# Performance work log

Measured on AMD Instinct MI355X. Metric: run time of the kernel, lower is better.

Reference implementation:

```python
import jax, jax.numpy as jnp
import numpy as np

D_MODEL, H, D_FF = 1024, 16, 4096
B, S = 2, 2048
EPS = 1e-6


def setup_inputs() -> dict:
    key = jax.random.key(0)
    ks = jax.random.split(key, 12)
    sc = 0.02
    p = lambda k, shape: (jax.random.normal(k, shape, dtype=jnp.float32) * sc)
    return {
        "x": jax.random.normal(ks[0], (B, S, D_MODEL), dtype=jnp.float32),
        "mask": jnp.ones((B, 1, 1, S), dtype=jnp.int32),
        "wq": p(ks[1], (D_MODEL, D_MODEL)), "bq": jnp.zeros((D_MODEL,), jnp.float32),
        "wk": p(ks[2], (D_MODEL, D_MODEL)), "bk": jnp.zeros((D_MODEL,), jnp.float32),
        "wv": p(ks[3], (D_MODEL, D_MODEL)), "bv": jnp.zeros((D_MODEL,), jnp.float32),
        "wo": p(ks[4], (D_MODEL, D_MODEL)), "bo": jnp.zeros((D_MODEL,), jnp.float32),
        "w1": p(ks[5], (D_FF, D_MODEL)), "b1": jnp.zeros((D_FF,), jnp.float32),
        "w2": p(ks[6], (D_MODEL, D_FF)), "b2": jnp.zeros((D_MODEL,), jnp.float32),
        "ln1_a": jnp.ones((D_MODEL,), jnp.float32), "ln1_b": jnp.zeros((D_MODEL,), jnp.float32),
        "ln2_a": jnp.ones((D_MODEL,), jnp.float32), "ln2_b": jnp.zeros((D_MODEL,), jnp.float32),
    }


def _layernorm(x, alpha, beta):
    # Matches the torch module: unbiased std (ddof=1), eps added to std (not var).
    mean = jnp.mean(x, axis=-1, keepdims=True)
    std = jnp.std(x, axis=-1, keepdims=True, ddof=1)
    return alpha * (x - mean) / (std + EPS) + beta


def _mha(x, mask, wq, bq, wk, bk, wv, bv, wo, bo):
    b, s, d = x.shape
    d_k = d // H
    # torch Linear: y = x @ W^T + b
    q = (x @ wq.T + bq).reshape(b, s, H, d_k).transpose(0, 2, 1, 3)
    k = (x @ wk.T + bk).reshape(b, s, H, d_k).transpose(0, 2, 1, 3)
    v = (x @ wv.T + bv).reshape(b, s, H, d_k).transpose(0, 2, 1, 3)
    scores = jnp.einsum("bhqd,bhkd->bhqk", q, k) / jnp.sqrt(jnp.float32(d_k))
    scores = jnp.where(mask == 0, jnp.float32(-1e9), scores)
    attn = jax.nn.softmax(scores, axis=-1)
    out = jnp.einsum("bhqk,bhkd->bhqd", attn, v)
    out = out.transpose(0, 2, 1, 3).reshape(b, s, d)
    return out @ wo.T + bo


def reference(x, mask, wq, bq, wk, bk, wv, bv, wo, bo, w1, b1, w2, b2,
              ln1_a, ln1_b, ln2_a, ln2_b):
    # Pre-LN MHA + residual
    h1 = _layernorm(x, ln1_a, ln1_b)
    x = x + _mha(h1, mask, wq, bq, wk, bk, wv, bv, wo, bo)
    # Pre-LN FFN + residual (dropout=0 -> identity)
    h2 = _layernorm(x, ln2_a, ln2_b)
    ff = jax.nn.relu(h2 @ w1.T + b1) @ w2.T + b2
    return x + ff
```

## Files before the change

kernel.cpp:

```cpp
#include <hip/hip_runtime.h>
#include <cstdint>
#include <cstddef>

typedef short bf16x8 __attribute__((ext_vector_type(8)));
typedef short bf16x4 __attribute__((ext_vector_type(4)));
typedef float f32x4 __attribute__((ext_vector_type(4)));

#define D_MODEL 1024
#define SEQ     2048
#define NBATCH  2
#define NH      16
#define DKH     64
#define DFF     4096
#define MROWS   (NBATCH * SEQ)

#if defined(__HIP_DEVICE_COMPILE__)
#if __has_builtin(__builtin_amdgcn_mfma_f32_16x16x16bf16_1k)
#define MFMA16(a, b, c) __builtin_amdgcn_mfma_f32_16x16x16bf16_1k(a, b, c, 0, 0, 0)
#else
#define MFMA16(a, b, c) __builtin_amdgcn_mfma_f32_16x16x16_bf16(a, b, c, 0, 0, 0)
#endif
#else
__device__ __host__ static inline f32x4 MFMA16(bf16x4, bf16x4, f32x4 c) {
  return c;
}
#endif

__device__ __forceinline__ unsigned short f2bf(float f) {
  unsigned u = __builtin_bit_cast(unsigned, f);
  u += 0x7fffu + ((u >> 16) & 1u);
  return (unsigned short)(u >> 16);
}
__device__ __forceinline__ unsigned packbf2(float lo, float hi) {
  unsigned r;
  asm("v_cvt_pk_bf16_f32 %0, %1, %2" : "=v"(r) : "v"(lo), "v"(hi));
  return r;
}
__device__ __forceinline__ void gload_lds16(const void* g, void* l) {
  __builtin_amdgcn_global_load_lds(
      (const __attribute__((address_space(1))) unsigned*)g,
      (__attribute__((address_space(3))) unsigned*)l, 16, 0, 0);
}

__global__ __launch_bounds__(256) void cast_weights_kernel(
    const float* __restrict__ wq, const float* __restrict__ wk,
    const float* __restrict__ wv, const float* __restrict__ wo,
    const float* __restrict__ w1, const float* __restrict__ w2,
    const int* __restrict__ mask, unsigned short* __restrict__ dst,
    float* __restrict__ maskf) {
  const int TOT4 = (12 << 20) >> 2;
  const int gid = blockIdx.x * blockDim.x + threadIdx.x;
  for (int i4 = gid; i4 < TOT4; i4 += gridDim.x * blockDim.x) {
    int i = i4 << 2;
    const float* src;
    int off;
    if (i < (4 << 20)) {
      src = (i < (2 << 20)) ? ((i < (1 << 20)) ? wq : wk)
                            : ((i < (3 << 20)) ? wv : wo);
      off = i & ((1 << 20) - 1);
    } else if (i < (8 << 20)) { src = w1; off = i - (4 << 20); }
    else                      { src = w2; off = i - (8 << 20); }
    float4 v = *(const float4*)(src + off);
    ushort4 o;
    o.x = f2bf(v.x); o.y = f2bf(v.y); o.z = f2bf(v.z); o.w = f2bf(v.w);
    *(ushort4*)(dst + i) = o;
  }
  if (gid < (NBATCH * SEQ / 4)) {
    int4 m = ((const int4*)mask)[gid];
    float4 f;
    f.x = (m.x == 0) ? -1e9f : 0.f;
    f.y = (m.y == 0) ? -1e9f : 0.f;
    f.z = (m.z == 0) ? -1e9f : 0.f;
    f.w = (m.w == 0) ? -1e9f : 0.f;
    ((float4*)maskf)[gid] = f;
  }
}

__global__ __launch_bounds__(256) void ln_kernel(
    const float* __restrict__ x, const float* __restrict__ alpha,
    const float* __restrict__ beta, unsigned short* __restrict__ out) {
  const int row = blockIdx.x;
  const int t = threadIdx.x;
  float4 v = *(const float4*)(x + (size_t)row * D_MODEL + t * 4);
  float s = v.x + v.y + v.z + v.w;
#pragma unroll
  for (int o = 1; o < 64; o <<= 1) s += __shfl_xor(s, o, 64);
  __shared__ float red[8];
  if ((t & 63) == 0) red[t >> 6] = s;
  __syncthreads();
  float mean = (red[0] + red[1] + red[2] + red[3]) * (1.f / D_MODEL);
  float dx = v.x - mean, dy = v.y - mean, dz = v.z - mean, dw = v.w - mean;
  float sq = dx * dx + dy * dy + dz * dz + dw * dw;
#pragma unroll
  for (int o = 1; o < 64; o <<= 1) sq += __shfl_xor(sq, o, 64);
  if ((t & 63) == 0) red[4 + (t >> 6)] = sq;
  __syncthreads();
  float var = (red[4] + red[5] + red[6] + red[7]) * (1.f / (D_MODEL - 1));
  float inv = 1.f / (sqrtf(var) + 1e-6f);
  float4 a = *(const float4*)(alpha + t * 4);
  float4 be = *(const float4*)(beta + t * 4);
  ushort4 o4;
  o4.x = f2bf(a.x * dx * inv + be.x);
  o4.y = f2bf(a.y * dy * inv + be.y);
  o4.z = f2bf(a.z * dz * inv + be.z);
  o4.w = f2bf(a.w * dw * inv + be.w);
  *(ushort4*)(out + (size_t)row * D_MODEL + t * 4) = o4;
}

#define GEMM_STAGE(A_, W_, LD_, koff_, kt_, buf_)                                  \
  {                                                                                \
    int ke_ = (koff_) + (kt_) * 32;                                                \
    gload_lds16(A_ + (size_t)(m0 + srow) * (LD_) + ke_ + sce, &lds[(buf_)][0][t * 8]);        \
    gload_lds16(A_ + (size_t)(m0 + 64 + srow) * (LD_) + ke_ + sce, &lds[(buf_)][0][2048 + t * 8]); \
    gload_lds16(W_ + (size_t)(n0 + srow) * (LD_) + ke_ + sce, &lds[(buf_)][1][t * 8]);        \
    gload_lds16(W_ + (size_t)(n0 + 64 + srow) * (LD_) + ke_ + sce, &lds[(buf_)][1][2048 + t * 8]); \
  }

#define GEMM_MAINLOOP(A_, W_, LD_, K_, koff_)                                      \
  GEMM_STAGE(A_, W_, LD_, koff_, 0, 0);                                            \
  for (int kt = 0; kt < ((K_) >> 5); ++kt) {                                       \
    __syncthreads();                                                               \
    if (kt + 1 < ((K_) >> 5)) GEMM_STAGE(A_, W_, LD_, koff_, kt + 1, (kt + 1) & 1); \
    const unsigned short* la = lds[kt & 1][0];                                     \
    const unsigned short* lb = lds[kt & 1][1];                                     \
    bf16x8 af[4], bfr[4];                                                          \
    _Pragma("unroll") for (int i = 0; i < 4; i++) {                                \
      af[i]  = *(const bf16x8*)&la[(wm + i * 16 + c) * 32 + g * 8];                \
      bfr[i] = *(const bf16x8*)&lb[(wn + i * 16 + c) * 32 + g * 8];                \
    }                                                                              \
    _Pragma("unroll") for (int mi = 0; mi < 4; mi++)                               \
      _Pragma("unroll") for (int ni = 0; ni < 4; ni++)                             \
        acc[mi][ni] = __builtin_amdgcn_mfma_f32_16x16x32_bf16(af[mi], bfr[ni],     \
                                                              acc[mi][ni], 0, 0, 0); \
  }

enum { MODE_BF16 = 0, MODE_RELU = 2, MODE_PARTIAL = 4 };

template <int MODE>
__global__ __launch_bounds__(256) void gemm_bt(
    const unsigned short* __restrict__ A, const unsigned short* __restrict__ W,
    const float* __restrict__ bias, void* __restrict__ outp, int M, int N, int K) {
  __shared__ unsigned short lds[2][2][128 * 32];
  const int t = threadIdx.x;
  const int lane = t & 63, wid = t >> 6;
  const int g = lane >> 4, c = lane & 15;
  const int m0 = blockIdx.y * 128, n0 = blockIdx.x * 128;
  const int wm = (wid >> 1) * 64, wn = (wid & 1) * 64;
  const int srow = t >> 2, sce = (t & 3) * 8;
  const int ldk = K * gridDim.z;
  const int koff = blockIdx.z * K;

  f32x4 zero = {0.f, 0.f, 0.f, 0.f};
  f32x4 acc[4][4];
#pragma unroll
  for (int i = 0; i < 4; i++)
#pragma unroll
    for (int j = 0; j < 4; j++) acc[i][j] = zero;

  GEMM_MAINLOOP(A, W, ldk, K, koff);

  float bv[4];
#pragma unroll
  for (int ni = 0; ni < 4; ni++)
    bv[ni] = (MODE == MODE_PARTIAL) ? 0.f : bias[n0 + wn + ni * 16 + c];

  float* po = (MODE == MODE_PARTIAL)
                  ? ((float*)outp + (size_t)blockIdx.z * M * N) : (float*)outp;

#pragma unroll
  for (int mi = 0; mi < 4; mi++) {
#pragma unroll
    for (int ni = 0; ni < 4; ni++) {
      const int mb = m0 + wm + mi * 16 + g * 4;
      const int n = n0 + wn + ni * 16 + c;
#pragma unroll
      for (int r = 0; r < 4; r++) {
        const int m = mb + r;
        float v = acc[mi][ni][r] + bv[ni];
        if (MODE == MODE_RELU) v = fmaxf(v, 0.f);
        if (MODE == MODE_PARTIAL) {
          po[(size_t)m * N + n] = v;
        } else {
          ((unsigned short*)outp)[(size_t)m * N + n] = f2bf(v);
        }
      }
    }
  }
}

__global__ __launch_bounds__(256) void gemm_qkv(
    const unsigned short* __restrict__ A, const unsigned short* __restrict__ Wbase,
    const float* __restrict__ bq, const float* __restrict__ bk,
    const float* __restrict__ bv_, unsigned short* __restrict__ qkout,
    unsigned short* __restrict__ vtout) {
  __shared__ unsigned short lds[2][2][128 * 32];
  const int t = threadIdx.x;
  const int lane = t & 63, wid = t >> 6;
  const int g = lane >> 4, c = lane & 15;
  const int wsel = blockIdx.x >> 3;
  const int m0 = blockIdx.y * 128, n0 = (blockIdx.x & 7) * 128;
  const int wm = (wid >> 1) * 64, wn = (wid & 1) * 64;
  const int srow = t >> 2, sce = (t & 3) * 8;
  const unsigned short* W = Wbase + ((size_t)wsel << 20);
  const float* bias = (wsel == 0) ? bq : (wsel == 1) ? bk : bv_;

  f32x4 zero = {0.f, 0.f, 0.f, 0.f};
  f32x4 acc[4][4];
#pragma unroll
  for (int i = 0; i < 4; i++)
#pragma unroll
    for (int j = 0; j < 4; j++) acc[i][j] = zero;

  GEMM_MAINLOOP(A, W, 1024, 1024, 0);

  float bvv[4];
#pragma unroll
  for (int ni = 0; ni < 4; ni++) bvv[ni] = bias[n0 + wn + ni * 16 + c];
  const float qsc = (wsel == 0) ? 0.125f : 1.f;

  if (wsel < 2) {
    unsigned short* outp = qkout + ((size_t)wsel << 22);
#pragma unroll
    for (int mi = 0; mi < 4; mi++) {
#pragma unroll
      for (int ni = 0; ni < 4; ni++) {
        const int mb = m0 + wm + mi * 16 + g * 4;
        const int n = n0 + wn + ni * 16 + c;
#pragma unroll
        for (int r = 0; r < 4; r++)
          outp[(size_t)(mb + r) * 1024 + n] = f2bf((acc[mi][ni][r] + bvv[ni]) * qsc);
      }
    }
  } else {
#pragma unroll
    for (int mi = 0; mi < 4; mi++) {
#pragma unroll
      for (int ni = 0; ni < 4; ni++) {
        const int mb = m0 + wm + mi * 16 + g * 4;
        const int n = n0 + wn + ni * 16 + c;
        const int b = mb >> 11, s2 = mb & 2047;
        ushort4 o4;
        o4.x = f2bf(acc[mi][ni][0] + bvv[ni]);
        o4.y = f2bf(acc[mi][ni][1] + bvv[ni]);
        o4.z = f2bf(acc[mi][ni][2] + bvv[ni]);
        o4.w = f2bf(acc[mi][ni][3] + bvv[ni]);
        *(ushort4*)(vtout + ((size_t)(b * 1024 + n)) * 2048 + s2) = o4;
      }
    }
  }
}

#define ATTN_STAGE64(base_, buf_)                                                   \
  {                                                                                 \
    const int r0_ = (t >> 3), r1_ = 32 + (t >> 3), ch_ = t & 7;                     \
    gload_lds16(Kb + (size_t)((base_) + r0_) * D_MODEL + ((ch_ ^ (r0_ & 7)) << 3),  \
                &Klds[buf_][t * 8]);                                                \
    gload_lds16(Kb + (size_t)((base_) + r1_) * D_MODEL + ((ch_ ^ (r1_ & 7)) << 3),  \
                &Klds[buf_][2048 + t * 8]);                                         \
    gload_lds16(Vb + (size_t)r0_ * SEQ + (base_) + ((ch_ ^ (r0_ & 7)) << 3),        \
                &Vlds[buf_][t * 8]);                                                \
    gload_lds16(Vb + (size_t)r1_ * SEQ + (base_) + ((ch_ ^ (r1_ & 7)) << 3),        \
                &Vlds[buf_][2048 + t * 8]);                                         \
  }

__global__ __launch_bounds__(256, 4) void attn_kernel(
    const unsigned short* __restrict__ Q, const unsigned short* __restrict__ Kmat,
    const unsigned short* __restrict__ Vt, const float* __restrict__ maskf,
    unsigned short* __restrict__ O) {
  __shared__ unsigned short Klds[2][64 * 64];
  __shared__ unsigned short Vlds[2][64 * 64];
  __shared__ float masklds[SEQ];
  const int t = threadIdx.x, lane = t & 63, wid = t >> 6;
  const int g = lane >> 4, c = lane & 15;
  const int bh = blockIdx.x, qt = blockIdx.y;
  const int b = bh >> 4, h = bh & 15;
  const int q0 = qt * 64 + wid * 16;

  const unsigned short* Qb = Q + (size_t)b * SEQ * D_MODEL + h * DKH;
  const unsigned short* Kb = Kmat + (size_t)b * SEQ * D_MODEL + h * DKH;
  const unsigned short* Vb = Vt + (size_t)bh * DKH * SEQ;
  const float* mbf = maskf + b * SEQ;

  bf16x8 qf[2];
#pragma unroll
  for (int kd = 0; kd < 2; kd++)
    qf[kd] = *(const bf16x8*)&Qb[(size_t)(q0 + c) * D_MODEL + kd * 32 + g * 8];

  f32x4 zero = {0.f, 0.f, 0.f, 0.f};
  f32x4 of[4];
#pragma unroll
  for (int j = 0; j < 4; j++) of[j] = zero;
  float mrun = -1e30f, lrun = 0.f;

  gload_lds16(mbf + t * 4, &masklds[t * 4]);
  gload_lds16(mbf + 1024 + t * 4, &masklds[1024 + t * 4]);
  ATTN_STAGE64(0, 0);

  for (int kv = 0; kv < 32; ++kv) {
    const int buf = kv & 1;
    const int base = kv * 64;
    __syncthreads();
    if (kv < 31) ATTN_STAGE64(base + 64, buf ^ 1);

    f32x4 sf[4];
    {
      bf16x8 kf0[4], kf1[4];
#pragma unroll
      for (int nb = 0; nb < 4; nb++) {
        const int row = nb * 16 + c;
        kf0[nb] = *(const bf16x8*)&Klds[buf][row * 64 + ((g ^ (c & 7)) << 3)];
        kf1[nb] = *(const bf16x8*)&Klds[buf][row * 64 + (((4 + g) ^ (c & 7)) << 3)];
      }
      __builtin_amdgcn_s_setprio(1);
#pragma unroll
      for (int nb = 0; nb < 4; nb++) {
        f32x4 s = zero;
        s = __builtin_amdgcn_mfma_f32_16x16x32_bf16(kf0[nb], qf[0], s, 0, 0, 0);
        s = __builtin_amdgcn_mfma_f32_16x16x32_bf16(kf1[nb], qf[1], s, 0, 0, 0);
        sf[nb] = s;
      }
      __builtin_amdgcn_s_setprio(0);
    }

#pragma unroll
    for (int nb = 0; nb < 4; nb++) {
      float4 ma = *(const float4*)&masklds[base + nb * 16 + g * 4];
      sf[nb][0] += ma.x; sf[nb][1] += ma.y; sf[nb][2] += ma.z; sf[nb][3] += ma.w;
    }

    float pm = -1e30f;
#pragma unroll
    for (int nb = 0; nb < 4; nb++)
#pragma unroll
      for (int r = 0; r < 4; r++) pm = fmaxf(pm, sf[nb][r]);
    pm = fmaxf(pm, __shfl_xor(pm, 16, 64));
    pm = fmaxf(pm, __shfl_xor(pm, 32, 64));
    if (!__all(pm <= mrun + 8.f)) {
      float mnew = fmaxf(mrun, pm);
      float fsc = exp2f((mrun - mnew) * 1.44269504f);
      lrun *= fsc;
#pragma unroll
      for (int dkb = 0; dkb < 4; dkb++) of[dkb] *= fsc;
      mrun = mnew;
    }
    const float mb2 = mrun * 1.44269504f;
    float ps = 0.f;
#pragma unroll
    for (int nb = 0; nb < 4; nb++)
#pragma unroll
      for (int r = 0; r < 4; r++) {
        float p = exp2f(fmaf(sf[nb][r], 1.44269504f, -mb2));
        sf[nb][r] = p;
        ps += p;
      }
    lrun += ps;

#pragma unroll
    for (int nb = 0; nb < 4; nb++) {
      bf16x4 vv[4];
#pragma unroll
      for (int dkb = 0; dkb < 4; dkb++) {
        const int row = dkb * 16 + c;
        const int vbyte = row * 128 + ((((nb << 1) + (g >> 1)) ^ (c & 7)) << 4) +
                          ((g & 1) << 3);
        vv[dkb] = *(const bf16x4*)((const char*)Vlds[buf] + vbyte);
      }
      unsigned plo = packbf2(sf[nb][0], sf[nb][1]);
      unsigned phi = packbf2(sf[nb][2], sf[nb][3]);
      unsigned long long uu = (unsigned long long)plo |
                              ((unsigned long long)phi << 32);
      bf16x4 pf = __builtin_bit_cast(bf16x4, uu);
      __builtin_amdgcn_s_setprio(1);
#pragma unroll
      for (int dkb = 0; dkb < 4; dkb++)
        of[dkb] = MFMA16(vv[dkb], pf, of[dkb]);
      __builtin_amdgcn_s_setprio(0);
    }
  }

  float lt = lrun;
  lt += __shfl_xor(lt, 16, 64);
  lt += __shfl_xor(lt, 32, 64);
  float inv = 1.f / lt;
#pragma unroll
  for (int dkb = 0; dkb < 4; dkb++) {
    ushort4 o4;
    o4.x = f2bf(of[dkb][0] * inv);
    o4.y = f2bf(of[dkb][1] * inv);
    o4.z = f2bf(of[dkb][2] * inv);
    o4.w = f2bf(of[dkb][3] * inv);
    *(ushort4*)&O[(size_t)(b * SEQ + q0 + c) * D_MODEL + h * DKH + dkb * 16 +
                  g * 4] = o4;
  }
}

__global__ __launch_bounds__(256) void proj_ln2_kernel(
    const float* __restrict__ x, const float* __restrict__ P0,
    const float* __restrict__ P1, const float* __restrict__ bo,
    const float* __restrict__ alpha, const float* __restrict__ beta,
    float* __restrict__ x2, unsigned short* __restrict__ h2) {
  const int row = blockIdx.x;
  const int t = threadIdx.x;
  const size_t idx = (size_t)row * D_MODEL + t * 4;
  float4 xv = *(const float4*)(x + idx);
  float4 p0 = *(const float4*)(P0 + idx);
  float4 p1 = *(const float4*)(P1 + idx);
  float4 bo4 = *(const float4*)(bo + t * 4);
  float4 v;
  v.x = xv.x + p0.x + p1.x + bo4.x;
  v.y = xv.y + p0.y + p1.y + bo4.y;
  v.z = xv.z + p0.z + p1.z + bo4.z;
  v.w = xv.w + p0.w + p1.w + bo4.w;
  *(float4*)(x2 + idx) = v;

  float s = v.x + v.y + v.z + v.w;
#pragma unroll
  for (int o = 1; o < 64; o <<= 1) s += __shfl_xor(s, o, 64);
  __shared__ float red[8];
  if ((t & 63) == 0) red[t >> 6] = s;
  __syncthreads();
  float mean = (red[0] + red[1] + red[2] + red[3]) * (1.f / D_MODEL);
  float dx = v.x - mean, dy = v.y - mean, dz = v.z - mean, dw = v.w - mean;
  float sq = dx * dx + dy * dy + dz * dz + dw * dw;
#pragma unroll
  for (int o = 1; o < 64; o <<= 1) sq += __shfl_xor(sq, o, 64);
  if ((t & 63) == 0) red[4 + (t >> 6)] = sq;
  __syncthreads();
  float var = (red[4] + red[5] + red[6] + red[7]) * (1.f / (D_MODEL - 1));
  float inv = 1.f / (sqrtf(var) + 1e-6f);
  float4 a = *(const float4*)(alpha + t * 4);
  float4 be = *(const float4*)(beta + t * 4);
  ushort4 o4;
  o4.x = f2bf(a.x * dx * inv + be.x);
  o4.y = f2bf(a.y * dy * inv + be.y);
  o4.z = f2bf(a.z * dz * inv + be.z);
  o4.w = f2bf(a.w * dw * inv + be.w);
  *(ushort4*)(h2 + idx) = o4;
}

__global__ __launch_bounds__(256) void ffn2_add_kernel(
    const float* __restrict__ x2, const float* __restrict__ Q0,
    const float* __restrict__ Q1, const float* __restrict__ b2,
    float* __restrict__ out) {
  const int i4 = blockIdx.x * blockDim.x + threadIdx.x;
  const size_t idx = (size_t)i4 * 4;
  float4 a = *(const float4*)(x2 + idx);
  float4 q0 = *(const float4*)(Q0 + idx);
  float4 q1 = *(const float4*)(Q1 + idx);
  float4 b = *(const float4*)(b2 + ((i4 & 255) * 4));
  float4 v;
  v.x = a.x + q0.x + q1.x + b.x;
  v.y = a.y + q0.y + q1.y + b.y;
  v.z = a.z + q0.z + q1.z + b.z;
  v.w = a.w + q0.w + q1.w + b.w;
  *(float4*)(out + idx) = v;
}

extern "C" void kernel_launch(void* const* d_in, const int* in_sizes, int n_in,
                              void* d_out, int out_size, void* d_ws, size_t ws_size,
                              hipStream_t stream) {
  (void)in_sizes; (void)n_in; (void)out_size; (void)ws_size;
  const float* x    = (const float*)d_in[0];
  const int*   mask = (const int*)d_in[1];
  const float* wq   = (const float*)d_in[2];
  const float* bq   = (const float*)d_in[3];
  const float* wk   = (const float*)d_in[4];
  const float* bk   = (const float*)d_in[5];
  const float* wv   = (const float*)d_in[6];
  const float* bv   = (const float*)d_in[7];
  const float* wo   = (const float*)d_in[8];
  const float* bo   = (const float*)d_in[9];
  const float* w1   = (const float*)d_in[10];
  const float* b1   = (const float*)d_in[11];
  const float* w2   = (const float*)d_in[12];
  const float* b2   = (const float*)d_in[13];
  const float* ln1a = (const float*)d_in[14];
  const float* ln1b = (const float*)d_in[15];
  const float* ln2a = (const float*)d_in[16];
  const float* ln2b = (const float*)d_in[17];

  char* ws = (char*)d_ws;
  unsigned short* w_bf  = (unsigned short*)ws;
  unsigned short* wq_bf = w_bf;
  unsigned short* wo_bf = w_bf + (3u << 20);
  unsigned short* w1_bf = w_bf + (4u << 20);
  unsigned short* w2_bf = w_bf + (8u << 20);
  unsigned short* h1    = (unsigned short*)(ws + (24u << 20));
  unsigned short* qbuf  = (unsigned short*)(ws + (32u << 20));
  unsigned short* kbuf  = (unsigned short*)(ws + (40u << 20));
  unsigned short* vtbuf = (unsigned short*)(ws + (48u << 20));
  unsigned short* attnb = (unsigned short*)(ws + (56u << 20));
  float*          x2    = (float*)(ws + (64u << 20));
  unsigned short* h2    = (unsigned short*)(ws + (80u << 20));
  unsigned short* ffn1  = (unsigned short*)(ws + (88u << 20));
  float*          pp    = (float*)(ws + (88u << 20));
  float*          qq    = (float*)(ws + (24u << 20));
  float*          maskf = (float*)(ws + (120u << 20));

  cast_weights_kernel<<<1024, 256, 0, stream>>>(wq, wk, wv, wo, w1, w2, mask,
                                                w_bf, maskf);
  ln_kernel<<<MROWS, 256, 0, stream>>>(x, ln1a, ln1b, h1);
  gemm_qkv<<<dim3(24, 32), 256, 0, stream>>>(h1, wq_bf, bq, bk, bv, qbuf, vtbuf);
  attn_kernel<<<dim3(32, 32), 256, 0, stream>>>(qbuf, kbuf, vtbuf, maskf, attnb);
  gemm_bt<MODE_PARTIAL><<<dim3(8, 32, 2), 256, 0, stream>>>(
      attnb, wo_bf, nullptr, (void*)pp, MROWS, D_MODEL, 512);
  proj_ln2_kernel<<<MROWS, 256, 0, stream>>>(
      x, pp, pp + (size_t)MROWS * D_MODEL, bo, ln2a, ln2b, x2, h2);
  gemm_bt<MODE_RELU><<<dim3(32, 32), 256, 0, stream>>>(
      h2, w1_bf, b1, (void*)ffn1, MROWS, DFF, D_MODEL);
  gemm_bt<MODE_PARTIAL><<<dim3(8, 32, 2), 256, 0, stream>>>(
      ffn1, w2_bf, nullptr, (void*)qq, MROWS, D_MODEL, 2048);
  ffn2_add_kernel<<<4096, 256, 0, stream>>>(
      x2, qq, qq + (size_t)MROWS * D_MODEL, b2, (float*)d_out);
}
```

Baseline: 275.7 us.

## Add 256x256-tile FFN1 GEMM with 16x16x32 MFMA and use raw exp2 intrinsic

Replaces the generic 128x128 ReLU GEMM for the first FFN layer with a dedicated 512-thread kernel. It uses 256x256 output tiles, double-buffered 64-wide K tiles loaded into LDS with XOR swizzle, and the 16x16x32 bf16 MFMA. The larger tiles and wider MFMA aim to raise operand reuse and cut LDS/global traffic per flop, at the cost of 128KB of LDS per block and a single wave of 256 blocks. Attention softmax also switches exp2f to the hardware exp2 builtin to drop range-handling overhead.

```diff
diff --git a/kernel.cpp b/kernel.cpp
--- a/kernel.cpp
+++ b/kernel.cpp
@@ -20,10 +20,16 @@
 #else
 #define MFMA16(a, b, c) __builtin_amdgcn_mfma_f32_16x16x16_bf16(a, b, c, 0, 0, 0)
 #endif
+#if __has_builtin(__builtin_amdgcn_exp2f)
+#define EXP2(x) __builtin_amdgcn_exp2f(x)
+#else
+#define EXP2(x) exp2f(x)
+#endif
 #else
 __device__ __host__ static inline f32x4 MFMA16(bf16x4, bf16x4, f32x4 c) {
   return c;
 }
+#define EXP2(x) exp2f(x)
 #endif
 
 __device__ __forceinline__ unsigned short f2bf(float f) {
@@ -188,6 +194,98 @@
   }
 }
 
+#define G256_STAGE(SRC_A, SRC_B, T_, b_)                                           \
+  {                                                                                \
+    _Pragma("unroll") for (int i_ = 0; i_ < 4; i_++) {                             \
+      const int r_ = srow + i_ * 64;                                               \
+      gload_lds16(SRC_A + (size_t)(m0 + r_) * K + (T_) * 64 +                      \
+                      ((sch ^ (r_ & 7)) << 3),                                     \
+                  &Atile[b_][r_ * 64 + sch * 8]);                                  \
+      gload_lds16(SRC_B + (size_t)(n0 + r_) * K + (T_) * 64 +                      \
+                      ((sch ^ (r_ & 7)) << 3),                                     \
+                  &Btile[b_][r_ * 64 + sch * 8]);                                  \
+    }                                                                              \
+  }
+
+__global__ __launch_bounds__(512, 2) void gemm256_relu(
+    const unsigned short* __restrict__ A, const unsigned short* __restrict__ W,
+    const float* __restrict__ bias, unsigned short* __restrict__ out,
+    int M, int N, int K) {
+  __shared__ unsigned short Atile[2][256 * 64];
+  __shared__ unsigned short Btile[2][256 * 64];
+  const int t = threadIdx.x, lane = t & 63, wid = t >> 6;
+  const int g = lane >> 4, c = lane & 15;
+  const int wr = wid >> 2, wc = wid & 3;
+  const int m0 = blockIdx.y * 256, n0 = blockIdx.x * 256;
+  const int srow = t >> 3, sch = t & 7;
+  const int NT = K >> 6;
+  (void)M;
+
+  f32x4 zero = {0.f, 0.f, 0.f, 0.f};
+  f32x4 acc[8][4];
+#pragma unroll
+  for (int i = 0; i < 8; i++)
+#pragma unroll
+    for (int j = 0; j < 4; j++) acc[i][j] = zero;
+
+  G256_STAGE(A, W, 0, 0);
+  G256_STAGE(A, W, 1, 1);
+
+  for (int T = 0; T < NT; ++T) {
+    const int b = T & 1;
+    if (T == 0) {
+      asm volatile("s_waitcnt vmcnt(8)" ::: "memory");
+    } else {
+      asm volatile("s_waitcnt vmcnt(0)" ::: "memory");
+    }
+    __builtin_amdgcn_sched_barrier(0);
+    __builtin_amdgcn_s_barrier();
+    if (T >= 1 && T + 1 < NT) G256_STAGE(A, W, T + 1, (T + 1) & 1);
+
+#pragma unroll
+    for (int q = 0; q < 4; ++q) {
+      const int kk = q >> 1, mh = (q & 1) * 4;
+      bf16x8 af[4], bfq[4];
+#pragma unroll
+      for (int j = 0; j < 4; j++) {
+        const int ar = wr * 128 + (mh + j) * 16 + c;
+        const int br = wc * 64 + j * 16 + c;
+        const int sl = ((kk * 4 + g) ^ (c & 7)) << 3;
+        af[j] = *(const bf16x8*)&Atile[b][ar * 64 + sl];
+        bfq[j] = *(const bf16x8*)&Btile[b][br * 64 + sl];
+      }
+      __builtin_amdgcn_s_barrier();
+      __builtin_amdgcn_s_setprio(1);
+#pragma unroll
+      for (int j = 0; j < 4; j++)
+#pragma unroll
+        for (int n = 0; n < 4; n++)
+          acc[mh + j][n] = __builtin_amdgcn_mfma_f32_16x16x32_bf16(
+              af[j], bfq[n], acc[mh + j][n], 0, 0, 0);
+      __builtin_amdgcn_s_setprio(0);
+      __builtin_amdgcn_s_barrier();
+    }
+  }
+
+  float bv[4];
+#pragma unroll
+  for (int ni = 0; ni < 4; ni++) bv[ni] = bias[n0 + wc * 64 + ni * 16 + c];
+
+#pragma unroll
+  for (int mi = 0; mi < 8; mi++) {
+#pragma unroll
+    for (int ni = 0; ni < 4; ni++) {
+      const int mb = m0 + wr * 128 + mi * 16 + g * 4;
+      const int n = n0 + wc * 64 + ni * 16 + c;
+#pragma unroll
+      for (int r = 0; r < 4; r++) {
+        float v = fmaxf(acc[mi][ni][r] + bv[ni], 0.f);
+        out[(size_t)(mb + r) * N + n] = f2bf(v);
+      }
+    }
+  }
+}
+
 __global__ __launch_bounds__(256) void gemm_qkv(
     const unsigned short* __restrict__ A, const unsigned short* __restrict__ Wbase,
     const float* __restrict__ bq, const float* __restrict__ bk,
@@ -337,7 +435,7 @@
     pm = fmaxf(pm, __shfl_xor(pm, 32, 64));
     if (!__all(pm <= mrun + 8.f)) {
       float mnew = fmaxf(mrun, pm);
-      float fsc = exp2f((mrun - mnew) * 1.44269504f);
+      float fsc = EXP2((mrun - mnew) * 1.44269504f);
       lrun *= fsc;
 #pragma unroll
       for (int dkb = 0; dkb < 4; dkb++) of[dkb] *= fsc;
@@ -349,7 +447,7 @@
     for (int nb = 0; nb < 4; nb++)
 #pragma unroll
       for (int r = 0; r < 4; r++) {
-        float p = exp2f(fmaf(sf[nb][r], 1.44269504f, -mb2));
+        float p = EXP2(fmaf(sf[nb][r], 1.44269504f, -mb2));
         sf[nb][r] = p;
         ps += p;
       }
@@ -506,8 +604,8 @@
       attnb, wo_bf, nullptr, (void*)pp, MROWS, D_MODEL, 512);
   proj_ln2_kernel<<<MROWS, 256, 0, stream>>>(
       x, pp, pp + (size_t)MROWS * D_MODEL, bo, ln2a, ln2b, x2, h2);
-  gemm_bt<MODE_RELU><<<dim3(32, 32), 256, 0, stream>>>(
-      h2, w1_bf, b1, (void*)ffn1, MROWS, DFF, D_MODEL);
+  gemm256_relu<<<dim3(16, 16), 512, 0, stream>>>(
+      h2, w1_bf, b1, ffn1, MROWS, DFF, D_MODEL);
   gemm_bt<MODE_PARTIAL><<<dim3(8, 32, 2), 256, 0, stream>>>(
       ffn1, w2_bf, nullptr, (void*)qq, MROWS, D_MODEL, 2048);
   ffn2_add_kernel<<<4096, 256, 0, stream>>>(
```

Result: faster. 262.7 us (-4.7%).
